# Performance work log

Measured on AMD Instinct MI355X. Metric: run time of the kernel, lower is better.

## Reference

```python
import jax, jax.numpy as jnp
import numpy as np

B, T, C, H = 4, 2048, 1024, 1024

def setup_inputs() -> dict:
    key = jax.random.key(0)
    ks = jax.random.split(key, 7)
    s = 0.02
    return {
        "x": jax.random.normal(ks[0], (B, T, C), dtype=jnp.float32),
        "k": jax.random.normal(ks[1], (B, T, C), dtype=jnp.float32),
        "q": jax.random.normal(ks[2], (B, T, C), dtype=jnp.float32),
        "v": jax.random.normal(ks[3], (B, T, C), dtype=jnp.float32),
        "Wk": jax.random.normal(ks[4], (C, H), dtype=jnp.float32) * s,
        "Wq": jax.random.normal(ks[5], (C, H), dtype=jnp.float32) * s,
        "Wv": jax.random.normal(ks[6], (C, H), dtype=jnp.float32) * s,
    }

def reference(x, k, q, v, Wk, Wq, Wv):
    Tcur = x.shape[1]
    kp = jnp.einsum('btc,ch->bth', k, Wk)
    qp = jnp.einsum('btc,ch->bth', q, Wq)
    # NOTE: original torch code (faithfully) projects v with the QUERY weights
    vp = jnp.einsum('btc,ch->bth', v, Wq)
    scale = jnp.asarray(H, jnp.float32) ** -0.5
    weights = jnp.einsum('bth,bsh->bts', qp, kp) * scale  # [B,T,T]
    causal = jnp.tril(jnp.ones((Tcur, Tcur), dtype=bool))
    weights = jnp.where(causal, weights, -jnp.inf)
    weights = jax.nn.softmax(weights, axis=-1)
    # dropout p=0.0 -> identity
    out = jnp.einsum('bts,bsh->bth', weights, vp)
    return out
```

## Files before the change

### kernel.cpp

```cpp
#include <hip/hip_runtime.h>
#include <stdint.h>
#include <math.h>

typedef unsigned short u16;
typedef __attribute__((ext_vector_type(8))) short short8;
typedef __attribute__((ext_vector_type(8))) u16 ushort8;
typedef __attribute__((ext_vector_type(4))) u16 u16x4;
typedef __attribute__((ext_vector_type(4))) float floatx4;

__device__ __forceinline__ u16 f2bf(float f) {
  union { float f; unsigned u; } c; c.f = f;
  unsigned u = c.u;
  return (u16)((u + 0x7fffu + ((u >> 16) & 1u)) >> 16);
}
__device__ __forceinline__ float bf2f(u16 h) {
  union { unsigned u; float f; } c; c.u = (unsigned)h << 16;
  return c.f;
}

__device__ __forceinline__ void async16(const u16* g, u16* l) {
  auto* gp = reinterpret_cast<const __attribute__((address_space(1))) uint32_t*>(
      reinterpret_cast<uintptr_t>(g));
  auto* lp = reinterpret_cast<__attribute__((address_space(3))) uint32_t*>(
      reinterpret_cast<uintptr_t>(l));
  __builtin_amdgcn_global_load_lds(gp, lp, 16, 0, 0);
}

#define WAIT_VM4 0xF74
#define WAIT_VM0 0xF70

template <int OUT_BF16>
__global__ __launch_bounds__(256) void gemm_bt(
    const u16* __restrict__ A, const u16* __restrict__ B, void* __restrict__ Cv,
    int K, int lda, int ldb, int ldc,
    long long sA, long long sB, long long sC,
    float scale, int tri_grid, int causal_klimit, int rev_m,
    int vpt, u16* __restrict__ vpC) {
  int bm, bn;
  if (tri_grid) {
    const int bx = blockIdx.x;
    int i = (int)((sqrtf(8.f * bx + 1.f) - 1.f) * 0.5f);
    while ((i + 1) * (i + 2) / 2 <= bx) ++i;
    while (i * (i + 1) / 2 > bx) --i;
    bm = i;
    bn = bx - i * (i + 1) / 2;
  } else {
    bm = rev_m ? ((int)gridDim.x - 1 - (int)blockIdx.x) : (int)blockIdx.x;
    bn = blockIdx.y;
  }
  const int m0 = bm * 128;
  const int n0 = bn * 128;
  A += (size_t)blockIdx.z * sA;
  B += (size_t)blockIdx.z * sB;

  __shared__ u16 As[2][4096];
  __shared__ u16 Bs[2][4096];

  const int tid = threadIdx.x;
  const int lane = tid & 63;
  const int wid = tid >> 6;
  const int wm = (wid & 1) * 64;
  const int wn = (wid >> 1) * 64;
  const int fr = lane & 15;
  const int fq = lane >> 4;

  floatx4 acc[4][4] = {};

  int kt_end = K >> 5;
  if (causal_klimit) {
    int lim = (m0 >> 5) + 4;
    if (lim < kt_end) kt_end = lim;
  }

  const int rowi = tid >> 2;
  const int segi = tid & 3;
  const int sgz = segi ^ ((rowi >> 1) & 3);
  const u16* gA = A + (size_t)(m0 + rowi) * lda + sgz * 8;
  const u16* gB = B + (size_t)(n0 + rowi) * ldb + sgz * 8;

  int offA[4], offB[4];
#pragma unroll
  for (int i = 0; i < 4; ++i) {
    int ra = wm + i * 16 + fr;
    offA[i] = ra * 32 + (fq ^ ((ra >> 1) & 3)) * 8;
    int rb = wn + i * 16 + fr;
    offB[i] = rb * 32 + (fq ^ ((rb >> 1) & 3)) * 8;
  }

  auto issue = [&](int kt) {
    const int k0 = kt << 5;
    const int odd = kt & 1;
    async16(gA + k0, &As[odd][tid * 8]);
    async16(gA + k0 + (size_t)64 * lda, &As[odd][tid * 8 + 2048]);
    async16(gB + k0, &Bs[odd][tid * 8]);
    async16(gB + k0 + (size_t)64 * ldb, &Bs[odd][tid * 8 + 2048]);
  };

  issue(0);
  for (int kt = 0; kt < kt_end; ++kt) {
    if (kt + 1 < kt_end) {
      issue(kt + 1);
      __builtin_amdgcn_s_waitcnt(WAIT_VM4);
    } else {
      __builtin_amdgcn_s_waitcnt(WAIT_VM0);
    }
    asm volatile("s_barrier" ::: "memory");

    const u16* ab = As[kt & 1];
    const u16* bb = Bs[kt & 1];
    short8 av[4], bv[4];
#pragma unroll
    for (int i = 0; i < 4; ++i) av[i] = *(const short8*)(ab + offA[i]);
#pragma unroll
    for (int j = 0; j < 4; ++j) bv[j] = *(const short8*)(bb + offB[j]);

#pragma unroll
    for (int i = 0; i < 4; ++i)
#pragma unroll
      for (int j = 0; j < 4; ++j)
        acc[i][j] = __builtin_amdgcn_mfma_f32_16x16x32_bf16(av[i], bv[j],
                                                            acc[i][j], 0, 0, 0);
    asm volatile("s_barrier" ::: "memory");
  }

  if (vpt && blockIdx.z == 2) {
#pragma unroll
    for (int i = 0; i < 4; ++i) {
      const int m = m0 + wm + i * 16 + fq * 4;
      const int b = m >> 11, t = m & 2047;
#pragma unroll
      for (int j = 0; j < 4; ++j) {
        const int n = n0 + wn + j * 16 + fr;
        u16x4 o;
#pragma unroll
        for (int r = 0; r < 4; ++r) o[r] = f2bf(acc[i][j][r]);
        *(u16x4*)&vpC[(size_t)b * 2097152 + (size_t)n * 2048 + t] = o;
      }
    }
    return;
  }
  if (OUT_BF16) {
    u16* C = (u16*)Cv + (size_t)blockIdx.z * sC;
#pragma unroll
    for (int i = 0; i < 4; ++i) {
      const int m = m0 + wm + i * 16 + fq * 4;
#pragma unroll
      for (int j = 0; j < 4; ++j) {
        const int n = n0 + wn + j * 16 + fr;
#pragma unroll
        for (int r = 0; r < 4; ++r)
          C[(size_t)(m + r) * ldc + n] = f2bf(acc[i][j][r] * scale);
      }
    }
  } else {
    float* C = (float*)Cv + (size_t)blockIdx.z * sC;
#pragma unroll
    for (int i = 0; i < 4; ++i) {
      const int m = m0 + wm + i * 16 + fq * 4;
#pragma unroll
      for (int j = 0; j < 4; ++j) {
        const int n = n0 + wn + j * 16 + fr;
#pragma unroll
        for (int r = 0; r < 4; ++r)
          C[(size_t)(m + r) * ldc + n] = acc[i][j][r] * scale;
      }
    }
  }
}

__global__ __launch_bounds__(256) void cast3(
    const float* __restrict__ q, const float* __restrict__ k,
    const float* __restrict__ v, u16* __restrict__ out, int n8) {
  int i = blockIdx.x * 256 + threadIdx.x;
  if (i >= n8) return;
  const float* src = blockIdx.y == 0 ? q : (blockIdx.y == 1 ? k : v);
  u16* dst = out + (size_t)blockIdx.y * n8 * 8;
  floatx4 a = ((const floatx4*)src)[i * 2];
  floatx4 b = ((const floatx4*)src)[i * 2 + 1];
  ushort8 o;
#pragma unroll
  for (int j = 0; j < 4; ++j) { o[j] = f2bf(a[j]); o[4 + j] = f2bf(b[j]); }
  ((ushort8*)dst)[i] = o;
}

__global__ __launch_bounds__(256) void transpose_castW(
    const float* __restrict__ Wq, const float* __restrict__ Wk,
    u16* __restrict__ out, int R, int C) {
  __shared__ u16 tile[64][72];
  const float* in = (blockIdx.z == 1) ? Wk : Wq;
  u16* dst = out + (size_t)blockIdx.z * R * C;
  const int r0 = blockIdx.x * 64;
  const int c0 = blockIdx.y * 64;
  const int tid = threadIdx.x;
#pragma unroll
  for (int rnd = 0; rnd < 2; ++rnd) {
    int e = rnd * 256 + tid;
    int rr = e >> 3, seg = e & 7;
    const float* p = &in[(size_t)(r0 + rr) * C + c0 + seg * 8];
    floatx4 a = *(const floatx4*)p;
    floatx4 b = *(const floatx4*)(p + 4);
    u16* tp = &tile[rr][seg * 8];
#pragma unroll
    for (int j = 0; j < 4; ++j) { tp[j] = f2bf(a[j]); tp[4 + j] = f2bf(b[j]); }
  }
  __syncthreads();
#pragma unroll
  for (int rnd = 0; rnd < 2; ++rnd) {
    int e = rnd * 256 + tid;
    int cc = e >> 3, rseg = e & 7;
    ushort8 tv;
#pragma unroll
    for (int j = 0; j < 8; ++j) tv[j] = tile[rseg * 8 + j][cc];
    *(ushort8*)&dst[(size_t)(c0 + cc) * R + r0 + rseg * 8] = tv;
  }
}

__global__ __launch_bounds__(256) void softmax_causal(u16* __restrict__ S,
                                                      int T) {
  const int row = blockIdx.x;
  const int t = row & (T - 1);
  const int len = t + 1;
  u16* srow = S + (size_t)row * T;
  const int tid = threadIdx.x;

  float vals[8];
  int cnt = 0;
  float mx = -1e30f;
  for (int i = tid; i < len; i += 256) {
    float v = bf2f(srow[i]);
    vals[cnt++] = v;
    mx = fmaxf(mx, v);
  }
  __shared__ float red[4];
#pragma unroll
  for (int o = 32; o > 0; o >>= 1) mx = fmaxf(mx, __shfl_down(mx, o, 64));
  if ((tid & 63) == 0) red[tid >> 6] = mx;
  __syncthreads();
  mx = fmaxf(fmaxf(red[0], red[1]), fmaxf(red[2], red[3]));
  __syncthreads();

  float sum = 0.f;
  for (int c = 0; c < cnt; ++c) {
    vals[c] = __expf(vals[c] - mx);
    sum += vals[c];
  }
#pragma unroll
  for (int o = 32; o > 0; o >>= 1) sum += __shfl_down(sum, o, 64);
  if ((tid & 63) == 0) red[tid >> 6] = sum;
  __syncthreads();
  sum = red[0] + red[1] + red[2] + red[3];
  const float inv = 1.f / sum;

  int c = 0;
  for (int i = tid; i < len; i += 256) srow[i] = f2bf(vals[c++] * inv);
  for (int i = tid; i < T; i += 256)
    if (i >= len) srow[i] = 0;
}

extern "C" void kernel_launch(void* const* d_in, const int* in_sizes, int n_in,
                              void* d_out, int out_size, void* d_ws,
                              size_t ws_size, hipStream_t stream) {
  (void)in_sizes; (void)n_in; (void)out_size; (void)ws_size;
  const float* k  = (const float*)d_in[1];
  const float* q  = (const float*)d_in[2];
  const float* v  = (const float*)d_in[3];
  const float* Wk = (const float*)d_in[4];
  const float* Wq = (const float*)d_in[5];
  float* out = (float*)d_out;

  const int B = 4, T = 2048, C = 1024, H = 1024;
  const int M = B * T;
  const size_t MC = (size_t)M * C, CH = (size_t)C * H, MH = (size_t)M * H;

  u16* qkv  = (u16*)d_ws;
  u16* WT   = qkv + 3 * MC;
  u16* qkvp = WT + 3 * CH;
  u16* vpT  = qkvp + 2 * MH;
  u16* Sb   = vpT + MH;

  const int n8 = (int)(MC / 8);
  cast3<<<dim3(n8 / 256, 3), 256, 0, stream>>>(q, k, v, qkv, n8);
  transpose_castW<<<dim3(C / 64, H / 64, 3), 256, 0, stream>>>(Wq, Wk, WT, C, H);

  gemm_bt<1><<<dim3(M / 128, H / 128, 3), 256, 0, stream>>>(
      qkv, WT, qkvp, C, C, C, H,
      (long long)MC, (long long)CH, (long long)MH, 1.f, 0, 0, 0, 1, vpT);

  gemm_bt<1><<<dim3(136, 1, B), 256, 0, stream>>>(
      qkvp, qkvp + MH, Sb, H, H, H, T,
      (long long)T * H, (long long)T * H, (long long)T * T,
      0.03125f, 1, 0, 0, 0, nullptr);

  softmax_causal<<<dim3(B * T), 256, 0, stream>>>(Sb, T);

  gemm_bt<0><<<dim3(T / 128, H / 128, B), 256, 0, stream>>>(
      Sb, vpT, out, T, T, T, H,
      (long long)T * T, (long long)H * T, (long long)T * H,
      1.f, 0, 1, 1, 0, nullptr);
}
```

Before: 332.8 us.

## Add 256x256-tile 8-wave GEMM for the QKV projection with pipelined staging

Adds a new bf16 MFMA GEMM kernel with 256x256 output tiles, 512 threads and a double-buffered LDS pipeline. Global loads for the next K-slices are interleaved between four MFMA sub-phases separated by barriers, and s_setprio raises priority during the MFMA sections. The projection GEMM launch now uses this kernel in place of the 128x128 version. The aim is more data reuse per LDS load and better overlap of memory traffic with compute. The cost is 128 KB of LDS per block and heavier register use, which limits occupancy.

```diff
diff --git a/kernel.cpp b/kernel.cpp
--- a/kernel.cpp
+++ b/kernel.cpp
@@ -168,6 +168,182 @@
   }
 }
 
+__global__ __launch_bounds__(512, 2) void gemm_bt_256(
+    const u16* __restrict__ A, const u16* __restrict__ B,
+    u16* __restrict__ Cb, int K, int lda, int ldb, int ldc,
+    long long sA, long long sB, long long sC, u16* __restrict__ vpC) {
+  const int m0 = blockIdx.x * 256;
+  const int n0 = blockIdx.y * 256;
+  A += (size_t)blockIdx.z * sA;
+  B += (size_t)blockIdx.z * sB;
+
+  __shared__ u16 lds[2][32768];
+
+  const int tid = threadIdx.x;
+  const int lane = tid & 63;
+  const int wid = tid >> 6;
+  const int wr = wid & 1;
+  const int wc = wid >> 1;
+  const int fr = lane & 15;
+  const int fq = lane >> 4;
+
+  floatx4 acc[8][4] = {};
+  const int NT = K >> 6;
+
+  const int srow = tid >> 3;
+  const int sseg = (tid & 7) ^ (srow & 7);
+  const u16* gA = A + (size_t)(m0 + srow) * lda + sseg * 8;
+  const u16* gB = B + (size_t)(n0 + srow) * ldb + sseg * 8;
+  const int ldst = tid * 8;
+
+  auto stageA = [&](int h, int t) {
+    u16* d = &lds[t & 1][h * 8192 + ldst];
+    const u16* s = gA + (size_t)(h * 128) * lda + t * 64;
+    async16(s, d);
+    async16(s + (size_t)64 * lda, d + 4096);
+  };
+  auto stageB = [&](int h, int t) {
+    u16* d = &lds[t & 1][16384 + h * 8192 + ldst];
+    const u16* s = gB + (size_t)(h * 128) * ldb + t * 64;
+    async16(s, d);
+    async16(s + (size_t)64 * ldb, d + 4096);
+  };
+
+  int aoff[2], boff[2];
+#pragma unroll
+  for (int s = 0; s < 2; ++s) {
+    const int seg = ((((s << 2) + fq) ^ (fr & 7))) * 8;
+    aoff[s] = wr * 8192 + fr * 64 + seg;
+    boff[s] = 16384 + (wc >> 1) * 8192 + (wc & 1) * 4096 + fr * 64 + seg;
+  }
+
+  stageA(0, 0); stageA(1, 0); stageB(0, 0); stageB(1, 0);
+  stageB(0, 1); stageB(1, 1);
+  __builtin_amdgcn_s_waitcnt(WAIT_VM4);
+  asm volatile("s_barrier" ::: "memory");
+
+  short8 a[4][2], b0[2][2], b1[2][2];
+  for (int t = 0; t < NT; ++t) {
+    const u16* L = lds[t & 1];
+
+#pragma unroll
+    for (int i = 0; i < 4; ++i)
+#pragma unroll
+      for (int s = 0; s < 2; ++s)
+        a[i][s] = *(const short8*)(L + aoff[s] + i * 1024);
+#pragma unroll
+    for (int j = 0; j < 2; ++j)
+#pragma unroll
+      for (int s = 0; s < 2; ++s)
+        b0[j][s] = *(const short8*)(L + boff[s] + j * 1024);
+    if (t + 1 < NT) stageA(0, t + 1);
+    asm volatile("s_barrier" ::: "memory");
+    __builtin_amdgcn_s_setprio(1);
+#pragma unroll
+    for (int i = 0; i < 4; ++i)
+#pragma unroll
+      for (int j = 0; j < 2; ++j) {
+        acc[i][j] = __builtin_amdgcn_mfma_f32_16x16x32_bf16(
+            a[i][0], b0[j][0], acc[i][j], 0, 0, 0);
+        acc[i][j] = __builtin_amdgcn_mfma_f32_16x16x32_bf16(
+            a[i][1], b0[j][1], acc[i][j], 0, 0, 0);
+      }
+    __builtin_amdgcn_s_setprio(0);
+    asm volatile("s_barrier" ::: "memory");
+
+#pragma unroll
+    for (int j = 0; j < 2; ++j)
+#pragma unroll
+      for (int s = 0; s < 2; ++s)
+        b1[j][s] = *(const short8*)(L + boff[s] + (2 + j) * 1024);
+    if (t + 1 < NT) stageA(1, t + 1);
+    asm volatile("s_barrier" ::: "memory");
+    __builtin_amdgcn_s_setprio(1);
+#pragma unroll
+    for (int i = 0; i < 4; ++i)
+#pragma unroll
+      for (int j = 0; j < 2; ++j) {
+        acc[i][2 + j] = __builtin_amdgcn_mfma_f32_16x16x32_bf16(
+            a[i][0], b1[j][0], acc[i][2 + j], 0, 0, 0);
+        acc[i][2 + j] = __builtin_amdgcn_mfma_f32_16x16x32_bf16(
+            a[i][1], b1[j][1], acc[i][2 + j], 0, 0, 0);
+      }
+    __builtin_amdgcn_s_setprio(0);
+    asm volatile("s_barrier" ::: "memory");
+
+#pragma unroll
+    for (int i = 0; i < 4; ++i)
+#pragma unroll
+      for (int s = 0; s < 2; ++s)
+        a[i][s] = *(const short8*)(L + aoff[s] + (4 + i) * 1024);
+    if (t + 2 < NT) stageB(0, t + 2);
+    asm volatile("s_barrier" ::: "memory");
+    __builtin_amdgcn_s_setprio(1);
+#pragma unroll
+    for (int i = 0; i < 4; ++i)
+#pragma unroll
+      for (int j = 0; j < 2; ++j) {
+        acc[4 + i][j] = __builtin_amdgcn_mfma_f32_16x16x32_bf16(
+            a[i][0], b0[j][0], acc[4 + i][j], 0, 0, 0);
+        acc[4 + i][j] = __builtin_amdgcn_mfma_f32_16x16x32_bf16(
+            a[i][1], b0[j][1], acc[4 + i][j], 0, 0, 0);
+      }
+    __builtin_amdgcn_s_setprio(0);
+    asm volatile("s_barrier" ::: "memory");
+
+    if (t + 2 < NT) {
+      stageB(1, t + 2);
+      __builtin_amdgcn_s_waitcnt(WAIT_VM4);
+    } else {
+      __builtin_amdgcn_s_waitcnt(WAIT_VM0);
+    }
+    asm volatile("s_barrier" ::: "memory");
+    __builtin_amdgcn_s_setprio(1);
+#pragma unroll
+    for (int i = 0; i < 4; ++i)
+#pragma unroll
+      for (int j = 0; j < 2; ++j) {
+        acc[4 + i][2 + j] = __builtin_amdgcn_mfma_f32_16x16x32_bf16(
+            a[i][0], b1[j][0], acc[4 + i][2 + j], 0, 0, 0);
+        acc[4 + i][2 + j] = __builtin_amdgcn_mfma_f32_16x16x32_bf16(
+            a[i][1], b1[j][1], acc[4 + i][2 + j], 0, 0, 0);
+      }
+    __builtin_amdgcn_s_setprio(0);
+    asm volatile("s_barrier" ::: "memory");
+  }
+
+  const int mBase = m0 + wr * 128;
+  const int nBase = n0 + wc * 64;
+  if (blockIdx.z == 2) {
+#pragma unroll
+    for (int i = 0; i < 8; ++i) {
+      const int m = mBase + i * 16 + fq * 4;
+      const int b = m >> 11, tt = m & 2047;
+#pragma unroll
+      for (int j = 0; j < 4; ++j) {
+        const int n = nBase + j * 16 + fr;
+        u16x4 o;
+#pragma unroll
+        for (int r = 0; r < 4; ++r) o[r] = f2bf(acc[i][j][r]);
+        *(u16x4*)&vpC[(size_t)b * 2097152 + (size_t)n * 2048 + tt] = o;
+      }
+    }
+  } else {
+    u16* Co = Cb + (size_t)blockIdx.z * sC;
+#pragma unroll
+    for (int i = 0; i < 8; ++i) {
+      const int m = mBase + i * 16 + fq * 4;
+#pragma unroll
+      for (int j = 0; j < 4; ++j) {
+        const int n = nBase + j * 16 + fr;
+#pragma unroll
+        for (int r = 0; r < 4; ++r)
+          Co[(size_t)(m + r) * ldc + n] = f2bf(acc[i][j][r]);
+      }
+    }
+  }
+}
+
 __global__ __launch_bounds__(256) void cast3(
     const float* __restrict__ q, const float* __restrict__ k,
     const float* __restrict__ v, u16* __restrict__ out, int n8) {
@@ -282,9 +458,9 @@
   cast3<<<dim3(n8 / 256, 3), 256, 0, stream>>>(q, k, v, qkv, n8);
   transpose_castW<<<dim3(C / 64, H / 64, 3), 256, 0, stream>>>(Wq, Wk, WT, C, H);
 
-  gemm_bt<1><<<dim3(M / 128, H / 128, 3), 256, 0, stream>>>(
+  gemm_bt_256<<<dim3(M / 256, H / 256, 3), 512, 0, stream>>>(
       qkv, WT, qkvp, C, C, C, H,
-      (long long)MC, (long long)CH, (long long)MH, 1.f, 0, 0, 0, 1, vpT);
+      (long long)MC, (long long)CH, (long long)MH, vpT);
 
   gemm_bt<1><<<dim3(136, 1, B), 256, 0, stream>>>(
       qkvp, qkvp + MH, Sb, H, H, H, T,
```

Result: no change. 338.2 us (+1.6%).
